# Kernel optimization log

Measured on AMD Instinct MI355X. Metric: run time of the kernel, lower is better.

Reference implementation:

```python
import jax, jax.numpy as jnp
import numpy as np
from jax import lax

NEG = -1e9  # stand-in for -inf that keeps gradients finite
T, V, L = 2048, 32000, 8


def setup_inputs() -> dict:
    key = jax.random.key(0)
    k1, k2, k3 = jax.random.split(key, 3)
    # log piece probabilities (valid distribution in log space)
    log_piece_probs = jax.nn.log_softmax(jax.random.normal(k1, (V,), dtype=jnp.float32))
    # match_idx[t, j] = vocab index of the (unique) piece matching sequence[t:t+j+1], or -1
    match_idx = jax.random.randint(k2, (T, L), 0, V, dtype=jnp.int32)
    keep = jax.random.uniform(k3, (T, L)) < 0.3
    keep = keep.at[:, 0].set(True)  # length-1 (single char) pieces always match -> segmentable
    in_range = (jnp.arange(T)[:, None] + jnp.arange(1, L + 1)[None, :]) <= T
    match_idx = jnp.where(keep & in_range, match_idx, -1)
    return {"log_piece_probs": log_piece_probs, "match_idx": match_idx}


def _forward(log_piece_probs, match_idx):
    T_, L_ = match_idx.shape
    V_ = log_piece_probs.shape[0]
    valid = match_idx >= 0
    # w[t, j] = log p(piece matching at pos t with length j+1), NEG if no match
    w = jnp.where(valid, log_piece_probs[jnp.clip(match_idx, 0)], NEG)  # [T, L]
    # wrev[r, j] = w[r - j, j]: contribution ending at position n = r+1 from length j+1
    wrev = jnp.stack(
        [jnp.pad(w[:, j], (j, 0), constant_values=NEG)[:T_] for j in range(L_)], axis=1
    )  # [T, L]

    # forward pass: alpha[n] = logsumexp_l alpha[n-l] + w[n-l, l-1], rolling buffer of last L alphas
    def astep(buf, wr):
        a = jax.nn.logsumexp(buf[::-1] + wr)  # buf[::-1][j] = alpha[n-1-j]
        return jnp.concatenate([buf[1:], a[None]]), a

    abuf0 = jnp.concatenate([jnp.full((L_ - 1,), NEG, jnp.float32), jnp.zeros((1,), jnp.float32)])
    _, a_rest = lax.scan(astep, abuf0, wrev)
    alpha = jnp.concatenate([jnp.zeros((1,), jnp.float32), a_rest])  # [T+1], alpha[0]=0

    # backward pass: beta[t] = logsumexp_l w[t, l-1] + beta[t+l], rolling buffer of next L betas
    def bstep(buf, wt):
        b = jax.nn.logsumexp(wt + buf)  # buf[j] = beta[t+1+j]
        return jnp.concatenate([b[None], buf[:-1]]), b

    bbuf0 = jnp.concatenate([jnp.zeros((1,), jnp.float32), jnp.full((L_ - 1,), NEG, jnp.float32)])
    _, b_rest = lax.scan(bstep, bbuf0, w, reverse=True)
    beta = jnp.concatenate([b_rest, jnp.zeros((1,), jnp.float32)])  # [T+1], beta[T]=0

    # posterior: P[t, i] = exp(alpha[t] + log p_i + beta[t+len] - alpha[T])
    nxt = jnp.arange(T_)[:, None] + jnp.arange(1, L_ + 1)[None, :]  # [T, L]
    beta_next = beta[jnp.clip(nxt, 0, T_)]
    logP = alpha[:T_, None] + w + beta_next - alpha[T_]
    vals = jnp.where(valid, jnp.exp(logP), 0.0)  # [T, L]
    P = jnp.zeros((T_, V_), jnp.float32).at[
        jnp.arange(T_)[:, None], jnp.clip(match_idx, 0)
    ].add(vals)
    return P


def reference(log_piece_probs, match_idx):
    return _forward(log_piece_probs, match_idx)
```

## Files before the change

kernel.cpp:

```cpp
#include <hip/hip_runtime.h>


#define NEGV -1e9f
#define LOG2E 1.4426950408889634f
constexpr int T = 2048;
constexpr int L = 8;
constexpr int V = 32000;
constexpr int NCH = 64;
constexpr int K = 32;
constexpr int BLK = 512;
constexpr int FILLB = 4096;
constexpr int N4 = T * V / 4;
constexpr int CH4 = N4 / FILLB;
constexpr int CPAD = K * 8 + 4;

__device__ __forceinline__ float hexp2(float x) { return __builtin_amdgcn_exp2f(x); }
__device__ __forceinline__ float hlog2(float x) { return __builtin_amdgcn_logf(x); }

__device__ __forceinline__ float lse8v(float t0, float t1, float t2, float t3,
                                       float t4, float t5, float t6, float t7) {
    float m = fmaxf(fmaxf(fmaxf(t0, t1), fmaxf(t2, t3)),
                    fmaxf(fmaxf(t4, t5), fmaxf(t6, t7)));
    float s = hexp2(t0 - m) + hexp2(t1 - m) + hexp2(t2 - m) + hexp2(t3 - m)
            + hexp2(t4 - m) + hexp2(t5 - m) + hexp2(t6 - m) + hexp2(t7 - m);
    return m + hlog2(s);
}

__global__ __launch_bounds__(BLK) void scan_fill_kernel(
        const float* __restrict__ logp, const int* __restrict__ midx,
        float* __restrict__ out, float* __restrict__ alpha, float* __restrict__ beta) {
    const int tid = threadIdx.x;
    const int bx = blockIdx.x;

    if (bx >= 2) {
        float4 z = make_float4(0.f, 0.f, 0.f, 0.f);
        float4* o4 = (float4*)out;
        const int base4 = (bx - 2) * CH4;
        const int end4 = base4 + CH4;
        for (int i = base4 + tid; i < end4; i += BLK) o4[i] = z;
        return;
    }

    __shared__ __align__(16) float sW[NCH * CPAD];
    __shared__ __align__(16) float sPm[NCH * 64];
    __shared__ float sVst[(NCH + 1) * 8];
    __shared__ float sOut[NCH * 33];

    if (bx == 0) {
        for (int o = tid; o < T * L; o += BLK) {
            int r = o >> 3, j = o & 7, t = r - j;
            float v = NEGV;
            if (t >= 0) { int m = midx[(t << 3) + j]; if (m >= 0) v = logp[m] * LOG2E; }
            sW[(r >> 5) * CPAD + (r & 31) * 8 + j] = v;
        }
    } else {
        for (int o = tid; o < T * L; o += BLK) {
            int s = o >> 3, j = o & 7, t = T - 1 - s;
            int m = midx[(t << 3) + j];
            sW[(s >> 5) * CPAD + (s & 31) * 8 + j] = (m >= 0) ? logp[m] * LOG2E : NEGV;
        }
    }
    __syncthreads();

    {
        const int c = tid >> 3, col = tid & 7;
        float q[8];
#pragma unroll
        for (int i = 0; i < 8; ++i) q[i] = (i == col) ? 0.f : NEGV;
        const float* wc = &sW[c * CPAD];
        float4 c0 = *(const float4*)(wc + 0), c1 = *(const float4*)(wc + 4);
        float4 b0 = *(const float4*)(wc + 8), b1 = *(const float4*)(wc + 12);
        for (int k = 0; k < K; ++k) {
            float4 a0, a1;
            if (k + 2 < K) {
                a0 = *(const float4*)(wc + (k + 2) * 8);
                a1 = *(const float4*)(wc + (k + 2) * 8 + 4);
            }
            float top = lse8v(c0.x + q[0], c0.y + q[1], c0.z + q[2], c0.w + q[3],
                              c1.x + q[4], c1.y + q[5], c1.z + q[6], c1.w + q[7]);
#pragma unroll
            for (int i = 7; i > 0; --i) q[i] = q[i - 1];
            q[0] = top;
            c0 = b0; c1 = b1; b0 = a0; b1 = a1;
        }
#pragma unroll
        for (int i = 0; i < 8; ++i) sPm[c * 64 + i * 8 + col] = q[i];
    }
    __syncthreads();

    if (tid < 8) {
        const int r = tid;
        float v = (r == 0) ? 0.f : NEGV;
        float4 r0 = *(const float4*)&sPm[r * 8];
        float4 r1 = *(const float4*)&sPm[r * 8 + 4];
        for (int cc = 0; cc < NCH; ++cc) {
            sVst[cc * 8 + r] = v;
            float4 n0, n1;
            if (cc + 1 < NCH) {
                n0 = *(const float4*)&sPm[(cc + 1) * 64 + r * 8];
                n1 = *(const float4*)&sPm[(cc + 1) * 64 + r * 8 + 4];
            }
            float vb0 = __shfl(v, 0, 8), vb1 = __shfl(v, 1, 8);
            float vb2 = __shfl(v, 2, 8), vb3 = __shfl(v, 3, 8);
            float vb4 = __shfl(v, 4, 8), vb5 = __shfl(v, 5, 8);
            float vb6 = __shfl(v, 6, 8), vb7 = __shfl(v, 7, 8);
            v = lse8v(r0.x + vb0, r0.y + vb1, r0.z + vb2, r0.w + vb3,
                      r1.x + vb4, r1.y + vb5, r1.z + vb6, r1.w + vb7);
            r0 = n0; r1 = n1;
        }
        sVst[NCH * 8 + r] = v;
    }
    __syncthreads();

    if (tid < NCH) {
        const int cc = tid;
        float ab[8];
#pragma unroll
        for (int i = 0; i < 8; ++i) ab[i] = sVst[cc * 8 + i];
        const float* wc = &sW[cc * CPAD];
        float4 c0 = *(const float4*)(wc + 0), c1 = *(const float4*)(wc + 4);
        float4 b0 = *(const float4*)(wc + 8), b1 = *(const float4*)(wc + 12);
        for (int k = 0; k < K; ++k) {
            float4 a0, a1;
            if (k + 2 < K) {
                a0 = *(const float4*)(wc + (k + 2) * 8);
                a1 = *(const float4*)(wc + (k + 2) * 8 + 4);
            }
            float val = lse8v(c0.x + ab[0], c0.y + ab[1], c0.z + ab[2], c0.w + ab[3],
                              c1.x + ab[4], c1.y + ab[5], c1.z + ab[6], c1.w + ab[7]);
            sOut[cc * 33 + k] = val;
#pragma unroll
            for (int i = 7; i > 0; --i) ab[i] = ab[i - 1];
            ab[0] = val;
            c0 = b0; c1 = b1; b0 = a0; b1 = a1;
        }
    }
    __syncthreads();

    if (bx == 0) {
        for (int o = tid; o < T; o += BLK)
            alpha[o + 1] = sOut[(o >> 5) * 33 + (o & 31)];
        if (tid == 0) alpha[0] = 0.f;
    } else {
        for (int o = tid; o < T; o += BLK) {
            int s = T - 1 - o;
            beta[o] = sOut[(s >> 5) * 33 + (s & 31)];
        }
        if (tid == 0) beta[T] = 0.f;
    }
}

__global__ __launch_bounds__(256) void scatter_kernel(
        const float* __restrict__ logp, const int* __restrict__ midx,
        float* __restrict__ out, const float* __restrict__ alpha,
        const float* __restrict__ beta) {
    int i = blockIdx.x * blockDim.x + threadIdx.x;
    if (i >= T * L) return;
    int m = midx[i];
    if (m < 0) return;
    int t = i >> 3, j = i & 7;
    int nx = t + j + 1;
    if (nx > T) nx = T;
    float lp2 = alpha[t] + logp[m] * LOG2E + beta[nx] - alpha[T];
    atomicAdd(&out[(size_t)t * V + m], hexp2(lp2));
}

extern "C" void kernel_launch(void* const* d_in, const int* in_sizes, int n_in,
                              void* d_out, int out_size, void* d_ws, size_t ws_size,
                              hipStream_t stream) {
    const float* logp = (const float*)d_in[0];
    const int*   midx = (const int*)d_in[1];
    float* out = (float*)d_out;

    float* ws    = (float*)d_ws;
    float* alpha = ws;
    float* beta  = alpha + 2064;

    scan_fill_kernel<<<dim3(2 + FILLB), BLK, 0, stream>>>(logp, midx, out, alpha, beta);
    scatter_kernel<<<dim3((T * L) / 256), 256, 0, stream>>>(logp, midx, out, alpha, beta);
}
```

Before: 287.0 us.

## Fuse scans, zero-fill and scatter into one kernel with hole-skipping fill

After: 365.3 us. +27.3%, slower.

```diff
diff --git a/kernel.cpp b/kernel.cpp
--- a/kernel.cpp
+++ b/kernel.cpp
@@ -9,9 +9,9 @@
 constexpr int NCH = 64;
 constexpr int K = 32;
 constexpr int BLK = 512;
-constexpr int FILLB = 4096;
-constexpr int N4 = T * V / 4;
-constexpr int CH4 = N4 / FILLB;
+constexpr int HALF = V / 2;
+constexpr int H4 = HALF / 4;
+constexpr int FILLB = 2 * T;
 constexpr int CPAD = K * 8 + 4;
 
 __device__ __forceinline__ float hexp2(float x) { return __builtin_amdgcn_exp2f(x); }
@@ -26,143 +26,182 @@
     return m + hlog2(s);
 }
 
-__global__ __launch_bounds__(BLK) void scan_fill_kernel(
+__global__ __launch_bounds__(BLK) void fused_kernel(
         const float* __restrict__ logp, const int* __restrict__ midx,
-        float* __restrict__ out, float* __restrict__ alpha, float* __restrict__ beta) {
+        float* __restrict__ out) {
     const int tid = threadIdx.x;
     const int bx = blockIdx.x;
-
-    if (bx >= 2) {
-        float4 z = make_float4(0.f, 0.f, 0.f, 0.f);
-        float4* o4 = (float4*)out;
-        const int base4 = (bx - 2) * CH4;
-        const int end4 = base4 + CH4;
-        for (int i = base4 + tid; i < end4; i += BLK) o4[i] = z;
-        return;
-    }
 
     __shared__ __align__(16) float sW[NCH * CPAD];
     __shared__ __align__(16) float sPm[NCH * 64];
     __shared__ float sVst[(NCH + 1) * 8];
-    __shared__ float sOut[NCH * 33];
-
-    if (bx == 0) {
-        for (int o = tid; o < T * L; o += BLK) {
-            int r = o >> 3, j = o & 7, t = r - j;
-            float v = NEGV;
-            if (t >= 0) { int m = midx[(t << 3) + j]; if (m >= 0) v = logp[m] * LOG2E; }
-            sW[(r >> 5) * CPAD + (r & 31) * 8 + j] = v;
-        }
-    } else {
-        for (int o = tid; o < T * L; o += BLK) {
-            int s = o >> 3, j = o & 7, t = T - 1 - s;
-            int m = midx[(t << 3) + j];
-            sW[(s >> 5) * CPAD + (s & 31) * 8 + j] = (m >= 0) ? logp[m] * LOG2E : NEGV;
-        }
+    __shared__ float sOutA[NCH * 33];
+    __shared__ float sOutB[NCH * 33];
+
+    if (bx > 0) {
+        const int idx = bx - 1;
+        const int t = idx >> 1;
+        const int half = idx & 1;
+        const int cbase = half * HALF;
+
+        int* sM = (int*)sW;
+        if (tid < 8) sM[tid] = midx[(t << 3) + tid];
+        __syncthreads();
+
+        int tcol[8], tf4[8];
+#pragma unroll
+        for (int j = 0; j < 8; ++j) {
+            int m = sM[j];
+            bool sp = (m >= cbase) && (m < cbase + HALF);
+            tcol[j] = sp ? (m - cbase) : -1;
+            tf4[j]  = sp ? (m - cbase) >> 2 : -1;
+        }
+
+        float4 z = make_float4(0.f, 0.f, 0.f, 0.f);
+        float4* o4 = (float4*)(out + (size_t)t * V + cbase);
+        for (int i = tid; i < H4; i += BLK) {
+            bool sp = false;
+#pragma unroll
+            for (int j = 0; j < 8; ++j) sp |= (i == tf4[j]);
+            if (!sp) {
+                o4[i] = z;
+            } else {
+                float* of = (float*)(o4 + i);
+#pragma unroll
+                for (int c = 0; c < 4; ++c) {
+                    int col = i * 4 + c;
+                    bool hit = false;
+#pragma unroll
+                    for (int j = 0; j < 8; ++j) hit |= (col == tcol[j]);
+                    if (!hit) of[c] = 0.f;
+                }
+            }
+        }
+        return;
     }
+
+    for (int pass = 0; pass < 2; ++pass) {
+        if (pass == 0) {
+            for (int o = tid; o < T * L; o += BLK) {
+                int r = o >> 3, j = o & 7, t = r - j;
+                float v = NEGV;
+                if (t >= 0) { int m = midx[(t << 3) + j]; if (m >= 0) v = logp[m] * LOG2E; }
+                sW[(r >> 5) * CPAD + (r & 31) * 8 + j] = v;
+            }
+        } else {
+            for (int o = tid; o < T * L; o += BLK) {
+                int s = o >> 3, j = o & 7, t = T - 1 - s;
+                int m = midx[(t << 3) + j];
+                sW[(s >> 5) * CPAD + (s & 31) * 8 + j] = (m >= 0) ? logp[m] * LOG2E : NEGV;
+            }
+        }
+        __syncthreads();
+
+        {
+            const int c = tid >> 3, col = tid & 7;
+            float q[8];
+#pragma unroll
+            for (int i = 0; i < 8; ++i) q[i] = (i == col) ? 0.f : NEGV;
+            const float* wc = &sW[c * CPAD];
+            float4 c0 = *(const float4*)(wc + 0), c1 = *(const float4*)(wc + 4);
+            float4 b0 = *(const float4*)(wc + 8), b1 = *(const float4*)(wc + 12);
+            for (int k = 0; k < K; ++k) {
+                float4 a0, a1;
+                if (k + 2 < K) {
+                    a0 = *(const float4*)(wc + (k + 2) * 8);
+                    a1 = *(const float4*)(wc + (k + 2) * 8 + 4);
+                }
+                float top = lse8v(c0.x + q[0], c0.y + q[1], c0.z + q[2], c0.w + q[3],
+                                  c1.x + q[4], c1.y + q[5], c1.z + q[6], c1.w + q[7]);
+#pragma unroll
+                for (int i = 7; i > 0; --i) q[i] = q[i - 1];
+                q[0] = top;
+                c0 = b0; c1 = b1; b0 = a0; b1 = a1;
+            }
+#pragma unroll
+            for (int i = 0; i < 8; ++i) sPm[c * 64 + i * 8 + col] = q[i];
+        }
+        __syncthreads();
+
+        if (tid < 8) {
+            const int r = tid;
+            float v = (r == 0) ? 0.f : NEGV;
+            float4 r0 = *(const float4*)&sPm[r * 8];
+            float4 r1 = *(const float4*)&sPm[r * 8 + 4];
+            for (int cc = 0; cc < NCH; ++cc) {
+                sVst[cc * 8 + r] = v;
+                float4 n0, n1;
+                if (cc + 1 < NCH) {
+                    n0 = *(const float4*)&sPm[(cc + 1) * 64 + r * 8];
+                    n1 = *(const float4*)&sPm[(cc + 1) * 64 + r * 8 + 4];
+                }
+                float vb0 = __shfl(v, 0, 8), vb1 = __shfl(v, 1, 8);
+                float vb2 = __shfl(v, 2, 8), vb3 = __shfl(v, 3, 8);
+                float vb4 = __shfl(v, 4, 8), vb5 = __shfl(v, 5, 8);
+                float vb6 = __shfl(v, 6, 8), vb7 = __shfl(v, 7, 8);
+                v = lse8v(r0.x + vb0, r0.y + vb1, r0.z + vb2, r0.w + vb3,
+                          r1.x + vb4, r1.y + vb5, r1.z + vb6, r1.w + vb7);
+                r0 = n0; r1 = n1;
+            }
+            sVst[NCH * 8 + r] = v;
+        }
+        __syncthreads();
+
+        {
+            float* so = pass ? sOutB : sOutA;
+            if (tid < NCH) {
+                const int cc = tid;
+                float ab[8];
+#pragma unroll
+                for (int i = 0; i < 8; ++i) ab[i] = sVst[cc * 8 + i];
+                const float* wc = &sW[cc * CPAD];
+                float4 c0 = *(const float4*)(wc + 0), c1 = *(const float4*)(wc + 4);
+                float4 b0 = *(const float4*)(wc + 8), b1 = *(const float4*)(wc + 12);
+                for (int k = 0; k < K; ++k) {
+                    float4 a0, a1;
+                    if (k + 2 < K) {
+                        a0 = *(const float4*)(wc + (k + 2) * 8);
+                        a1 = *(const float4*)(wc + (k + 2) * 8 + 4);
+                    }
+                    float val = lse8v(c0.x + ab[0], c0.y + ab[1], c0.z + ab[2], c0.w + ab[3],
+                                      c1.x + ab[4], c1.y + ab[5], c1.z + ab[6], c1.w + ab[7]);
+                    so[cc * 33 + k] = val;
+#pragma unroll
+                    for (int i = 7; i > 0; --i) ab[i] = ab[i - 1];
+                    ab[0] = val;
+                    c0 = b0; c1 = b1; b0 = a0; b1 = a1;
+                }
+            }
+        }
+        __syncthreads();
+    }
+
+
+    int* sM = (int*)sW;
+    for (int o = tid; o < T * L; o += BLK) sM[o] = midx[o];
     __syncthreads();
 
-    {
-        const int c = tid >> 3, col = tid & 7;
-        float q[8];
-#pragma unroll
-        for (int i = 0; i < 8; ++i) q[i] = (i == col) ? 0.f : NEGV;
-        const float* wc = &sW[c * CPAD];
-        float4 c0 = *(const float4*)(wc + 0), c1 = *(const float4*)(wc + 4);
-        float4 b0 = *(const float4*)(wc + 8), b1 = *(const float4*)(wc + 12);
-        for (int k = 0; k < K; ++k) {
-            float4 a0, a1;
-            if (k + 2 < K) {
-                a0 = *(const float4*)(wc + (k + 2) * 8);
-                a1 = *(const float4*)(wc + (k + 2) * 8 + 4);
-            }
-            float top = lse8v(c0.x + q[0], c0.y + q[1], c0.z + q[2], c0.w + q[3],
-                              c1.x + q[4], c1.y + q[5], c1.z + q[6], c1.w + q[7]);
-#pragma unroll
-            for (int i = 7; i > 0; --i) q[i] = q[i - 1];
-            q[0] = top;
-            c0 = b0; c1 = b1; b0 = a0; b1 = a1;
-        }
-#pragma unroll
-        for (int i = 0; i < 8; ++i) sPm[c * 64 + i * 8 + col] = q[i];
+    const float aT = sOutA[((T - 1) >> 5) * 33 + ((T - 1) & 31)];
+    for (int o = tid; o < T * L; o += BLK) {
+        int t = o >> 3, j = o & 7;
+        int m = sM[o];
+        if (m < 0) continue;
+        const int rb = t << 3;
+        bool lowest = true;
+        for (int jj = 0; jj < j; ++jj) lowest &= (sM[rb + jj] != m);
+        if (!lowest) continue;
+        float a_t = (t == 0) ? 0.f : sOutA[((t - 1) >> 5) * 33 + ((t - 1) & 31)];
+        float lp = logp[m] * LOG2E;
+        float s = 0.f;
+        for (int jj = j; jj < 8; ++jj) {
+            if (sM[rb + jj] != m) continue;
+            int nx = t + jj + 1; if (nx > T) nx = T;
+            float b = (nx == T) ? 0.f
+                                : sOutB[((T - 1 - nx) >> 5) * 33 + ((T - 1 - nx) & 31)];
+            s += hexp2(a_t + lp + b - aT);
+        }
+        out[(size_t)t * V + m] = s;
     }
-    __syncthreads();
-
-    if (tid < 8) {
-        const int r = tid;
-        float v = (r == 0) ? 0.f : NEGV;
-        float4 r0 = *(const float4*)&sPm[r * 8];
-        float4 r1 = *(const float4*)&sPm[r * 8 + 4];
-        for (int cc = 0; cc < NCH; ++cc) {
-            sVst[cc * 8 + r] = v;
-            float4 n0, n1;
-            if (cc + 1 < NCH) {
-                n0 = *(const float4*)&sPm[(cc + 1) * 64 + r * 8];
-                n1 = *(const float4*)&sPm[(cc + 1) * 64 + r * 8 + 4];
-            }
-            float vb0 = __shfl(v, 0, 8), vb1 = __shfl(v, 1, 8);
-            float vb2 = __shfl(v, 2, 8), vb3 = __shfl(v, 3, 8);
-            float vb4 = __shfl(v, 4, 8), vb5 = __shfl(v, 5, 8);
-            float vb6 = __shfl(v, 6, 8), vb7 = __shfl(v, 7, 8);
-            v = lse8v(r0.x + vb0, r0.y + vb1, r0.z + vb2, r0.w + vb3,
-                      r1.x + vb4, r1.y + vb5, r1.z + vb6, r1.w + vb7);
-            r0 = n0; r1 = n1;
-        }
-        sVst[NCH * 8 + r] = v;
-    }
-    __syncthreads();
-
-    if (tid < NCH) {
-        const int cc = tid;
-        float ab[8];
-#pragma unroll
-        for (int i = 0; i < 8; ++i) ab[i] = sVst[cc * 8 + i];
-        const float* wc = &sW[cc * CPAD];
-        float4 c0 = *(const float4*)(wc + 0), c1 = *(const float4*)(wc + 4);
-        float4 b0 = *(const float4*)(wc + 8), b1 = *(const float4*)(wc + 12);
-        for (int k = 0; k < K; ++k) {
-            float4 a0, a1;
-            if (k + 2 < K) {
-                a0 = *(const float4*)(wc + (k + 2) * 8);
-                a1 = *(const float4*)(wc + (k + 2) * 8 + 4);
-            }
-            float val = lse8v(c0.x + ab[0], c0.y + ab[1], c0.z + ab[2], c0.w + ab[3],
-                              c1.x + ab[4], c1.y + ab[5], c1.z + ab[6], c1.w + ab[7]);
-            sOut[cc * 33 + k] = val;
-#pragma unroll
-            for (int i = 7; i > 0; --i) ab[i] = ab[i - 1];
-            ab[0] = val;
-            c0 = b0; c1 = b1; b0 = a0; b1 = a1;
-        }
-    }
-    __syncthreads();
-
-    if (bx == 0) {
-        for (int o = tid; o < T; o += BLK)
-            alpha[o + 1] = sOut[(o >> 5) * 33 + (o & 31)];
-        if (tid == 0) alpha[0] = 0.f;
-    } else {
-        for (int o = tid; o < T; o += BLK) {
-            int s = T - 1 - o;
-            beta[o] = sOut[(s >> 5) * 33 + (s & 31)];
-        }
-        if (tid == 0) beta[T] = 0.f;
-    }
-}
-
-__global__ __launch_bounds__(256) void scatter_kernel(
-        const float* __restrict__ logp, const int* __restrict__ midx,
-        float* __restrict__ out, const float* __restrict__ alpha,
-        const float* __restrict__ beta) {
-    int i = blockIdx.x * blockDim.x + threadIdx.x;
-    if (i >= T * L) return;
-    int m = midx[i];
-    if (m < 0) return;
-    int t = i >> 3, j = i & 7;
-    int nx = t + j + 1;
-    if (nx > T) nx = T;
-    float lp2 = alpha[t] + logp[m] * LOG2E + beta[nx] - alpha[T];
-    atomicAdd(&out[(size_t)t * V + m], hexp2(lp2));
 }
 
 extern "C" void kernel_launch(void* const* d_in, const int* in_sizes, int n_in,
@@ -172,10 +211,5 @@
     const int*   midx = (const int*)d_in[1];
     float* out = (float*)d_out;
 
-    float* ws    = (float*)d_ws;
-    float* alpha = ws;
-    float* beta  = alpha + 2064;
-
-    scan_fill_kernel<<<dim3(2 + FILLB), BLK, 0, stream>>>(logp, midx, out, alpha, beta);
-    scatter_kernel<<<dim3((T * L) / 256), 256, 0, stream>>>(logp, midx, out, alpha, beta);
+    fused_kernel<<<dim3(1 + FILLB), BLK, 0, stream>>>(logp, midx, out);
 }
```

## Fuse output zero-fill with posterior scatter per row, dropping atomics

Applied to the files above, without the earlier changes.

Result: slower. 296.4 us (+3.3%).

```diff
diff --git a/kernel.cpp b/kernel.cpp
--- a/kernel.cpp
+++ b/kernel.cpp
@@ -9,10 +9,8 @@
 constexpr int NCH = 64;
 constexpr int K = 32;
 constexpr int BLK = 512;
-constexpr int FILLB = 4096;
-constexpr int N4 = T * V / 4;
-constexpr int CH4 = N4 / FILLB;
 constexpr int CPAD = K * 8 + 4;
+constexpr int R4 = V / 4;
 
 __device__ __forceinline__ float hexp2(float x) { return __builtin_amdgcn_exp2f(x); }
 __device__ __forceinline__ float hlog2(float x) { return __builtin_amdgcn_logf(x); }
@@ -26,20 +24,11 @@
     return m + hlog2(s);
 }
 
-__global__ __launch_bounds__(BLK) void scan_fill_kernel(
+__global__ __launch_bounds__(BLK) void scan_kernel(
         const float* __restrict__ logp, const int* __restrict__ midx,
-        float* __restrict__ out, float* __restrict__ alpha, float* __restrict__ beta) {
+        float* __restrict__ alpha, float* __restrict__ beta) {
     const int tid = threadIdx.x;
     const int bx = blockIdx.x;
-
-    if (bx >= 2) {
-        float4 z = make_float4(0.f, 0.f, 0.f, 0.f);
-        float4* o4 = (float4*)out;
-        const int base4 = (bx - 2) * CH4;
-        const int end4 = base4 + CH4;
-        for (int i = base4 + tid; i < end4; i += BLK) o4[i] = z;
-        return;
-    }
 
     __shared__ __align__(16) float sW[NCH * CPAD];
     __shared__ __align__(16) float sPm[NCH * 64];
@@ -150,19 +139,54 @@
     }
 }
 
-__global__ __launch_bounds__(256) void scatter_kernel(
+__global__ __launch_bounds__(256) void fill_scatter_kernel(
         const float* __restrict__ logp, const int* __restrict__ midx,
         float* __restrict__ out, const float* __restrict__ alpha,
         const float* __restrict__ beta) {
-    int i = blockIdx.x * blockDim.x + threadIdx.x;
-    if (i >= T * L) return;
-    int m = midx[i];
-    if (m < 0) return;
-    int t = i >> 3, j = i & 7;
-    int nx = t + j + 1;
-    if (nx > T) nx = T;
-    float lp2 = alpha[t] + logp[m] * LOG2E + beta[nx] - alpha[T];
-    atomicAdd(&out[(size_t)t * V + m], hexp2(lp2));
+    const int t = blockIdx.x;
+    const int tid = threadIdx.x;
+
+    int m[8];
+    float lp[8], bt[8], a_t = 0.f, aT = 0.f;
+    if (tid == 0) {
+        int4 r0 = ((const int4*)(midx + (t << 3)))[0];
+        int4 r1 = ((const int4*)(midx + (t << 3)))[1];
+        m[0] = r0.x; m[1] = r0.y; m[2] = r0.z; m[3] = r0.w;
+        m[4] = r1.x; m[5] = r1.y; m[6] = r1.z; m[7] = r1.w;
+        a_t = alpha[t];
+        aT = alpha[T];
+#pragma unroll
+        for (int j = 0; j < 8; ++j) {
+            int mm = m[j] < 0 ? 0 : m[j];
+            lp[j] = logp[mm];
+            int nx = t + j + 1; if (nx > T) nx = T;
+            bt[j] = beta[nx];
+        }
+    }
+
+    float4 z = make_float4(0.f, 0.f, 0.f, 0.f);
+    float4* o4 = (float4*)(out + (size_t)t * V);
+    for (int i = tid; i < R4; i += 256) o4[i] = z;
+
+    __syncthreads();
+
+    if (tid == 0) {
+#pragma unroll
+        for (int j = 0; j < 8; ++j) {
+            if (m[j] < 0) continue;
+            bool lowest = true;
+#pragma unroll
+            for (int jj = 0; jj < 8; ++jj)
+                if (jj < j) lowest &= (m[jj] != m[j]);
+            if (!lowest) continue;
+            float s = 0.f;
+#pragma unroll
+            for (int jj = 0; jj < 8; ++jj)
+                if (jj >= j && m[jj] == m[j])
+                    s += hexp2(a_t + lp[jj] * LOG2E + bt[jj] - aT);
+            out[(size_t)t * V + m[j]] = s;
+        }
+    }
 }
 
 extern "C" void kernel_launch(void* const* d_in, const int* in_sizes, int n_in,
@@ -176,6 +200,6 @@
     float* alpha = ws;
     float* beta  = alpha + 2064;
 
-    scan_fill_kernel<<<dim3(2 + FILLB), BLK, 0, stream>>>(logp, midx, out, alpha, beta);
-    scatter_kernel<<<dim3((T * L) / 256), 256, 0, stream>>>(logp, midx, out, alpha, beta);
-}
+    scan_kernel<<<dim3(2), BLK, 0, stream>>>(logp, midx, alpha, beta);
+    fill_scatter_kernel<<<dim3(T), 256, 0, stream>>>(logp, midx, out, alpha, beta);
+}
```

## Fuse forward/backward scans and scatter into one block; zero-fill in separate kernel

Applied to the files above, without the earlier changes.

New measurement: 312.3 us. 8.8% more time.

```diff
diff --git a/kernel.cpp b/kernel.cpp
--- a/kernel.cpp
+++ b/kernel.cpp
@@ -8,14 +8,15 @@
 constexpr int V = 32000;
 constexpr int NCH = 64;
 constexpr int K = 32;
-constexpr int BLK = 512;
-constexpr int FILLB = 4096;
-constexpr int N4 = T * V / 4;
-constexpr int CH4 = N4 / FILLB;
 constexpr int CPAD = K * 8 + 4;
+constexpr int R4 = V / 4;
 
 __device__ __forceinline__ float hexp2(float x) { return __builtin_amdgcn_exp2f(x); }
 __device__ __forceinline__ float hlog2(float x) { return __builtin_amdgcn_logf(x); }
+
+__device__ __forceinline__ int swa(int t, int j) {
+    return ((t >> 5) * CPAD) + ((t & 31) << 3) + j;
+}
 
 __device__ __forceinline__ float lse8v(float t0, float t1, float t2, float t3,
                                        float t4, float t5, float t6, float t7) {
@@ -26,79 +27,74 @@
     return m + hlog2(s);
 }
 
-__global__ __launch_bounds__(BLK) void scan_fill_kernel(
+__global__ __launch_bounds__(256) void fill_kernel(float* __restrict__ out) {
+    const int t = blockIdx.x;
+    float4 z = make_float4(0.f, 0.f, 0.f, 0.f);
+    float4* o4 = (float4*)(out + (size_t)t * V);
+    for (int i = threadIdx.x; i < R4; i += 256) o4[i] = z;
+}
+
+__global__ __launch_bounds__(1024) void scan_scatter_kernel(
         const float* __restrict__ logp, const int* __restrict__ midx,
-        float* __restrict__ out, float* __restrict__ alpha, float* __restrict__ beta) {
+        float* __restrict__ out) {
     const int tid = threadIdx.x;
-    const int bx = blockIdx.x;
-
-    if (bx >= 2) {
-        float4 z = make_float4(0.f, 0.f, 0.f, 0.f);
-        float4* o4 = (float4*)out;
-        const int base4 = (bx - 2) * CH4;
-        const int end4 = base4 + CH4;
-        for (int i = base4 + tid; i < end4; i += BLK) o4[i] = z;
-        return;
-    }
+    const int half = tid >> 9;
+    const int tl = tid & 511;
 
     __shared__ __align__(16) float sW[NCH * CPAD];
-    __shared__ __align__(16) float sPm[NCH * 64];
-    __shared__ float sVst[(NCH + 1) * 8];
-    __shared__ float sOut[NCH * 33];
+    __shared__ __align__(16) float sPm[2][NCH * 64];
+    __shared__ float sVst[2][NCH * 8];
+    __shared__ float sOut[2][NCH * 33];
 
-    if (bx == 0) {
-        for (int o = tid; o < T * L; o += BLK) {
-            int r = o >> 3, j = o & 7, t = r - j;
-            float v = NEGV;
-            if (t >= 0) { int m = midx[(t << 3) + j]; if (m >= 0) v = logp[m] * LOG2E; }
-            sW[(r >> 5) * CPAD + (r & 31) * 8 + j] = v;
-        }
-    } else {
-        for (int o = tid; o < T * L; o += BLK) {
-            int s = o >> 3, j = o & 7, t = T - 1 - s;
-            int m = midx[(t << 3) + j];
-            sW[(s >> 5) * CPAD + (s & 31) * 8 + j] = (m >= 0) ? logp[m] * LOG2E : NEGV;
-        }
+    for (int o = tid; o < T * L; o += 1024) {
+        int m = midx[o];
+        sW[swa(o >> 3, o & 7)] = (m >= 0) ? logp[m] * LOG2E : NEGV;
     }
     __syncthreads();
 
     {
-        const int c = tid >> 3, col = tid & 7;
+        const int c = tl >> 3, col = tl & 7;
         float q[8];
 #pragma unroll
         for (int i = 0; i < 8; ++i) q[i] = (i == col) ? 0.f : NEGV;
-        const float* wc = &sW[c * CPAD];
-        float4 c0 = *(const float4*)(wc + 0), c1 = *(const float4*)(wc + 4);
-        float4 b0 = *(const float4*)(wc + 8), b1 = *(const float4*)(wc + 12);
         for (int k = 0; k < K; ++k) {
-            float4 a0, a1;
-            if (k + 2 < K) {
-                a0 = *(const float4*)(wc + (k + 2) * 8);
-                a1 = *(const float4*)(wc + (k + 2) * 8 + 4);
+            float v[8];
+            if (half == 0) {
+                int r = c * K + k;
+#pragma unroll
+                for (int j = 0; j < 8; ++j) {
+                    int t = r - j;
+                    v[j] = (t >= 0) ? sW[swa(t, j)] : NEGV;
+                }
+            } else {
+                int t = T - 1 - (c * K + k);
+                float4 r0 = *(const float4*)&sW[swa(t, 0)];
+                float4 r1 = *(const float4*)&sW[swa(t, 4)];
+                v[0] = r0.x; v[1] = r0.y; v[2] = r0.z; v[3] = r0.w;
+                v[4] = r1.x; v[5] = r1.y; v[6] = r1.z; v[7] = r1.w;
             }
-            float top = lse8v(c0.x + q[0], c0.y + q[1], c0.z + q[2], c0.w + q[3],
-                              c1.x + q[4], c1.y + q[5], c1.z + q[6], c1.w + q[7]);
+            float top = lse8v(v[0] + q[0], v[1] + q[1], v[2] + q[2], v[3] + q[3],
+                              v[4] + q[4], v[5] + q[5], v[6] + q[6], v[7] + q[7]);
 #pragma unroll
             for (int i = 7; i > 0; --i) q[i] = q[i - 1];
             q[0] = top;
-            c0 = b0; c1 = b1; b0 = a0; b1 = a1;
         }
 #pragma unroll
-        for (int i = 0; i < 8; ++i) sPm[c * 64 + i * 8 + col] = q[i];
+        for (int i = 0; i < 8; ++i) sPm[half][c * 64 + i * 8 + col] = q[i];
     }
     __syncthreads();
 
-    if (tid < 8) {
-        const int r = tid;
+    if (tl < 8) {
+        const int r = tl;
         float v = (r == 0) ? 0.f : NEGV;
-        float4 r0 = *(const float4*)&sPm[r * 8];
-        float4 r1 = *(const float4*)&sPm[r * 8 + 4];
+        float4 r0 = *(const float4*)&sPm[half][r * 8];
+        float4 r1 = *(const float4*)&sPm[half][r * 8 + 4];
         for (int cc = 0; cc < NCH; ++cc) {
-            sVst[cc * 8 + r] = v;
+            sVst[half][cc * 8 + r] = v;
             float4 n0, n1;
             if (cc + 1 < NCH) {
-                n0 = *(const float4*)&sPm[(cc + 1) * 64 + r * 8];
-                n1 = *(const float4*)&sPm[(cc + 1) * 64 + r * 8 + 4];
+                n0 = *(const float4*)&sPm[half][(cc + 1) * 64 + r * 8];
+                n1 = *(const float4*)&sPm[half][(cc + 1) * 64 + r * 8 + 4];
             }
             float vb0 = __shfl(v, 0, 8), vb1 = __shfl(v, 1, 8);
             float vb2 = __shfl(v, 2, 8), vb3 = __shfl(v, 3, 8);
@@ -108,61 +104,57 @@
                       r1.x + vb4, r1.y + vb5, r1.z + vb6, r1.w + vb7);
             r0 = n0; r1 = n1;
         }
-        sVst[NCH * 8 + r] = v;
     }
     __syncthreads();
 
-    if (tid < NCH) {
-        const int cc = tid;
+    if (tl < NCH) {
+        const int cc = tl;
         float ab[8];
 #pragma unroll
-        for (int i = 0; i < 8; ++i) ab[i] = sVst[cc * 8 + i];
-        const float* wc = &sW[cc * CPAD];
-        float4 c0 = *(const float4*)(wc + 0), c1 = *(const float4*)(wc + 4);
-        float4 b0 = *(const float4*)(wc + 8), b1 = *(const float4*)(wc + 12);
+        for (int i = 0; i < 8; ++i) ab[i] = sVst[half][cc * 8 + i];
         for (int k = 0; k < K; ++k) {
-            float4 a0, a1;
-            if (k + 2 < K) {
-                a0 = *(const float4*)(wc + (k + 2) * 8);
-                a1 = *(const float4*)(wc + (k + 2) * 8 + 4);
+            float v[8];
+            if (half == 0) {
+                int r = cc * K + k;
+#pragma unroll
+                for (int j = 0; j < 8; ++j) {
+                    int t = r - j;
+                    v[j] = (t >= 0) ? sW[swa(t, j)] : NEGV;
+                }
+            } else {
+                int t = T - 1 - (cc * K + k);
+                float4 r0 = *(const float4*)&sW[swa(t, 0)];
+                float4 r1 = *(const float4*)&sW[swa(t, 4)];
+                v[0] = r0.x; v[1] = r0.y; v[2] = r0.z; v[3] = r0.w;
+                v[4] = r1.x; v[5] = r1.y; v[6] = r1.z; v[7] = r1.w;
             }
-            float val = lse8v(c0.x + ab[0], c0.y + ab[1], c0.z + ab[2], c0.w + ab[3],
-                              c1.x + ab[4], c1.y + ab[5], c1.z + ab[6], c1.w + ab[7]);
-            sOut[cc * 33 + k] = val;
+            float val = lse8v(v[0] + ab[0], v[1] + ab[1], v[2] + ab[2], v[3] + ab[3],
+                              v[4] + ab[4], v[5] + ab[5], v[6] + ab[6], v[7] + ab[7]);
+            sOut[half][cc * 33 + k] = val;
 #pragma unroll
             for (int i = 7; i > 0; --i) ab[i] = ab[i - 1];
             ab[0] = val;
-            c0 = b0; c1 = b1; b0 = a0; b1 = a1;
         }
     }
     __syncthreads();
 
-    if (bx == 0) {
-        for (int o = tid; o < T; o += BLK)
-            alpha[o + 1] = sOut[(o >> 5) * 33 + (o & 31)];
-        if (tid == 0) alpha[0] = 0.f;
-    } else {
-        for (int o = tid; o < T; o += BLK) {
-            int s = T - 1 - o;
-            beta[o] = sOut[(s >> 5) * 33 + (s & 31)];
+
+    const float aT = sOut[0][((T - 1) >> 5) * 33 + ((T - 1) & 31)];
+    for (int o = tid; o < T * L; o += 1024) {
+        int m = midx[o];
+        if (m < 0) continue;
+        int t = o >> 3, j = o & 7;
+        int nx = t + j + 1;
+        if (nx > T) nx = T;
+        float a = (t == 0) ? 0.f : sOut[0][((t - 1) >> 5) * 33 + ((t - 1) & 31)];
+        float b = 0.f;
+        if (nx < T) {
+            int s = T - 1 - nx;
+            b = sOut[1][(s >> 5) * 33 + (s & 31)];
         }
-        if (tid == 0) beta[T] = 0.f;
+        float w2 = sW[swa(t, j)];
+        atomicAdd(&out[(size_t)t * V + m], hexp2(a + w2 + b - aT));
     }
-}
-
-__global__ __launch_bounds__(256) void scatter_kernel(
-        const float* __restrict__ logp, const int* __restrict__ midx,
-        float* __restrict__ out, const float* __restrict__ alpha,
-        const float* __restrict__ beta) {
-    int i = blockIdx.x * blockDim.x + threadIdx.x;
-    if (i >= T * L) return;
-    int m = midx[i];
-    if (m < 0) return;
-    int t = i >> 3, j = i & 7;
-    int nx = t + j + 1;
-    if (nx > T) nx = T;
-    float lp2 = alpha[t] + logp[m] * LOG2E + beta[nx] - alpha[T];
-    atomicAdd(&out[(size_t)t * V + m], hexp2(lp2));
 }
 
 extern "C" void kernel_launch(void* const* d_in, const int* in_sizes, int n_in,
@@ -172,10 +164,6 @@
     const int*   midx = (const int*)d_in[1];
     float* out = (float*)d_out;
 
-    float* ws    = (float*)d_ws;
-    float* alpha = ws;
-    float* beta  = alpha + 2064;
-
-    scan_fill_kernel<<<dim3(2 + FILLB), BLK, 0, stream>>>(logp, midx, out, alpha, beta);
-    scatter_kernel<<<dim3((T * L) / 256), 256, 0, stream>>>(logp, midx, out, alpha, beta);
+    fill_kernel<<<dim3(T), 256, 0, stream>>>(out);
+    scan_scatter_kernel<<<dim3(1), 1024, 0, stream>>>(logp, midx, out);
 }
```
